# Kernel optimization log

Hardware: AMD Instinct MI355X
Metric: run time of the kernel (lower is better)

Reference implementation:

```python
import jax, jax.numpy as jnp
import numpy as np

HIDDEN = 1152
N_HEADS = 4
N_KV = 1
HEAD_DIM = 256
EPS = 1e-6
B, S = 4, 2048
ROPE_THETA = 1000000.0


def _rms_norm(x, w):
    # x: [..., D] float32; Gemma-style (1 + w) scale
    xf = x.astype(jnp.float32)
    inv = jax.lax.rsqrt(jnp.mean(xf * xf, axis=-1, keepdims=True) + EPS)
    return (xf * inv * (1.0 + w.astype(jnp.float32))).astype(x.dtype)


def _apply_rope(x, cos, sin):
    # x: [B, H, S, D]; cos/sin: [S, D/2]
    d2 = x.shape[-1] // 2
    x1, x2 = x[..., :d2], x[..., d2:]
    cos = cos[None, None, :, :]
    sin = sin[None, None, :, :]
    xr = x1 * cos - x2 * sin
    xi = x1 * sin + x2 * cos
    return jnp.concatenate([xr, xi], axis=-1).astype(x.dtype)


def setup_inputs() -> dict:
    key = jax.random.key(0)
    k_h, k_qkv, k_qn, k_kn, k_o = jax.random.split(key, 5)
    hidden_states = jax.random.normal(k_h, (B, S, HIDDEN), dtype=jnp.float32)
    # causal additive mask [1,1,S,S]
    neg = jnp.finfo(jnp.float32).min
    causal = jnp.tril(jnp.ones((S, S), dtype=bool))
    attention_mask = jnp.where(causal, 0.0, neg)[None, None, :, :].astype(jnp.float32)
    # RoPE tables (complex freqs_cis split into cos/sin)
    inv_freq = 1.0 / (ROPE_THETA ** (np.arange(0, HEAD_DIM, 2, dtype=np.float32) / HEAD_DIM))
    ang = np.arange(S, dtype=np.float32)[:, None] * inv_freq[None, :]
    freqs_cos = jnp.asarray(np.cos(ang))
    freqs_sin = jnp.asarray(np.sin(ang))
    qkv_out = (N_HEADS + 2 * N_KV) * HEAD_DIM
    scale = HIDDEN ** -0.5
    w_qkv = jax.random.normal(k_qkv, (HIDDEN, qkv_out), dtype=jnp.float32) * scale
    w_o = jax.random.normal(k_o, (N_HEADS * HEAD_DIM, HIDDEN), dtype=jnp.float32) * (N_HEADS * HEAD_DIM) ** -0.5
    q_norm_w = jax.random.normal(k_qn, (HEAD_DIM,), dtype=jnp.float32) * 0.02
    k_norm_w = jax.random.normal(k_kn, (HEAD_DIM,), dtype=jnp.float32) * 0.02
    return {
        "hidden_states": hidden_states,
        "attention_mask": attention_mask,
        "freqs_cos": freqs_cos,
        "freqs_sin": freqs_sin,
        "w_qkv": w_qkv,
        "q_norm_w": q_norm_w,
        "k_norm_w": k_norm_w,
        "w_o": w_o,
    }


def reference(hidden_states, attention_mask, freqs_cos, freqs_sin, w_qkv, q_norm_w, k_norm_w, w_o):
    b, s, _ = hidden_states.shape
    groups = N_HEADS // N_KV
    scaling = HEAD_DIM ** -0.5

    qkv = jnp.einsum("bsh,ho->bso", hidden_states, w_qkv)
    q_end = N_HEADS * HEAD_DIM
    k_end = q_end + N_KV * HEAD_DIM
    q = qkv[:, :, :q_end].reshape(b, s, N_HEADS, HEAD_DIM).transpose(0, 2, 1, 3)
    k = qkv[:, :, q_end:k_end].reshape(b, s, N_KV, HEAD_DIM).transpose(0, 2, 1, 3)
    v = qkv[:, :, k_end:].reshape(b, s, N_KV, HEAD_DIM).transpose(0, 2, 1, 3)

    q = _rms_norm(q, q_norm_w)
    k = _rms_norm(k, k_norm_w)

    q = _apply_rope(q, freqs_cos, freqs_sin)
    k = _apply_rope(k, freqs_cos, freqs_sin)

    if groups > 1:
        k = jnp.repeat(k, groups, axis=1)  # [B, H, S, D]
        v = jnp.repeat(v, groups, axis=1)

    scores = jnp.einsum("bhqd,bhkd->bhqk", q * scaling, k)
    scores = scores + attention_mask.astype(jnp.float32)
    probs = jax.nn.softmax(scores.astype(jnp.float32), axis=-1).astype(q.dtype)

    attn = jnp.einsum("bhqk,bhkd->bhqd", probs, v)
    attn = attn.transpose(0, 2, 1, 3).reshape(b, s, N_HEADS * HEAD_DIM)
    return jnp.einsum("bsf,fh->bsh", attn, w_o)
```

## Files before the change

### kernel.cpp

```cpp
#include <hip/hip_runtime.h>

typedef _Float16 f16;
typedef _Float16 f16x8 __attribute__((ext_vector_type(8)));
typedef _Float16 f16x4 __attribute__((ext_vector_type(4)));
typedef float f32x4 __attribute__((ext_vector_type(4)));

#define NH 4
#define HD 256
#define BB 4
#define SS 2048
#define HID 1152
#define QKV_N 1536
#define ODIM (NH * HD)

#define QKV16_OFF 0L
#define HID16_OFF 25165824L
#define OBUF_OFF 0L
#define OPART_OFF 16777216L
#define ML_OFF 44040192L
#define QB_OFF 50331648L
#define KB_OFF 67108864L
#define VT_OFF 71303168L
#define WQKVT_OFF 75497472L
#define WOT_OFF 79036416L

#define GLL16(gp, lp)                                                      \
  __builtin_amdgcn_global_load_lds(                                       \
      (const __attribute__((address_space(1))) char*)(gp),                \
      (__attribute__((address_space(3))) char*)(lp), 16, 0, 0)

__global__ __launch_bounds__(256) void cvt_f32_to_f16(
    const float* __restrict__ s, f16* __restrict__ d, long n) {
  long i = ((long)blockIdx.x * 256 + threadIdx.x) * 8;
  long stride = (long)gridDim.x * 256 * 8;
  for (; i < n; i += stride) {
    float4 a = *(const float4*)(s + i);
    float4 b = *(const float4*)(s + i + 4);
    f16x8 h = {(f16)a.x, (f16)a.y, (f16)a.z, (f16)a.w,
               (f16)b.x, (f16)b.y, (f16)b.z, (f16)b.w};
    *(f16x8*)(d + i) = h;
  }
}

template <typename ST>
__global__ __launch_bounds__(256) void transpose_cvt(
    const ST* __restrict__ src, long src_ld, long src_bs,
    f16* __restrict__ dst, long dst_ld, long dst_bs) {
  __shared__ float tile[32][33];
  src += (long)blockIdx.z * src_bs;
  dst += (long)blockIdx.z * dst_bs;
  int r0 = blockIdx.y * 32, c0 = blockIdx.x * 32;
  int tc = threadIdx.x & 31, tr = threadIdx.x >> 5;
#pragma unroll
  for (int i = 0; i < 4; ++i)
    tile[tr + i * 8][tc] = (float)src[(long)(r0 + tr + i * 8) * src_ld + c0 + tc];
  __syncthreads();
#pragma unroll
  for (int i = 0; i < 4; ++i)
    dst[(long)(c0 + tr + i * 8) * dst_ld + r0 + tc] = (f16)tile[tc][tr + i * 8];
}

template <typename CT>
__global__ __launch_bounds__(256, 3) void gemm_f16(
    const f16* __restrict__ A, const f16* __restrict__ Bt,
    CT* __restrict__ C, int K, int N) {
  __shared__ f16 As[128][64];
  __shared__ f16 Bs[128][64];
  int tid = threadIdx.x, wave = tid >> 6, lane = tid & 63;
  int l16 = lane & 15, lhi = lane >> 4;
  int wm = (wave >> 1) * 64, wn = (wave & 1) * 64;
  long bm = (long)blockIdx.x * 128, bn = (long)blockIdx.y * 128;
  f32x4 acc[4][4] = {};

  int srow = wave * 32 + (lane >> 3);
  int scol = (lane & 7) * 8;
  const f16* Ag = A + (bm + srow) * (long)K + scol;
  const f16* Bg = Bt + (bn + srow) * (long)K + scol;

  for (int k0 = 0; k0 < K; k0 += 64) {
#pragma unroll
    for (int i = 0; i < 4; ++i)
      GLL16(Ag + k0 + (long)i * 8 * K, &As[wave * 32 + i * 8][0]);
#pragma unroll
    for (int i = 0; i < 4; ++i)
      GLL16(Bg + k0 + (long)i * 8 * K, &Bs[wave * 32 + i * 8][0]);
    __syncthreads();
#pragma unroll
    for (int kb = 0; kb < 2; ++kb) {
      f16x8 af[4], bf[4];
#pragma unroll
      for (int i = 0; i < 4; ++i)
        af[i] = *(const f16x8*)&As[wm + i * 16 + l16][kb * 32 + lhi * 8];
#pragma unroll
      for (int j = 0; j < 4; ++j)
        bf[j] = *(const f16x8*)&Bs[wn + j * 16 + l16][kb * 32 + lhi * 8];
#pragma unroll
      for (int i = 0; i < 4; ++i)
#pragma unroll
        for (int j = 0; j < 4; ++j)
          acc[i][j] =
              __builtin_amdgcn_mfma_f32_16x16x32_f16(bf[j], af[i], acc[i][j], 0, 0, 0);
    }
    __syncthreads();
  }

#pragma unroll
  for (int i = 0; i < 4; ++i) {
    long m = bm + wm + i * 16 + l16;
#pragma unroll
    for (int j = 0; j < 4; ++j) {
      long n = bn + wn + j * 16 + lhi * 4;
      if constexpr (sizeof(CT) == 2) {
        f16x4 h = {(f16)acc[i][j][0], (f16)acc[i][j][1], (f16)acc[i][j][2],
                   (f16)acc[i][j][3]};
        *(f16x4*)&C[m * N + n] = h;
      } else {
        *(f32x4*)&C[m * N + n] = acc[i][j];
      }
    }
  }
}

__device__ __forceinline__ void norm_rope_store(
    const f16* __restrict__ x, const float* __restrict__ w,
    const float* __restrict__ fc, const float* __restrict__ fs,
    f16* __restrict__ dst, float scale, int lane) {
  float x0 = (float)x[lane], x1 = (float)x[lane + 64];
  float x2 = (float)x[lane + 128], x3 = (float)x[lane + 192];
  float ss = x0 * x0 + x1 * x1 + x2 * x2 + x3 * x3;
#pragma unroll
  for (int m = 1; m < 64; m <<= 1) ss += __shfl_xor(ss, m, 64);
  float inv = rsqrtf(ss * (1.0f / 256.0f) + 1e-6f);
  x0 *= inv * (1.0f + w[lane]);
  x1 *= inv * (1.0f + w[lane + 64]);
  x2 *= inv * (1.0f + w[lane + 128]);
  x3 *= inv * (1.0f + w[lane + 192]);
  float c0 = fc[lane], s0 = fs[lane], c1 = fc[lane + 64], s1 = fs[lane + 64];
  dst[lane]       = (f16)((x0 * c0 - x2 * s0) * scale);
  dst[lane + 64]  = (f16)((x1 * c1 - x3 * s1) * scale);
  dst[lane + 128] = (f16)((x0 * s0 + x2 * c0) * scale);
  dst[lane + 192] = (f16)((x1 * s1 + x3 * c1) * scale);
}

__global__ __launch_bounds__(256) void qkv_post(
    const f16* __restrict__ qkv, const float* __restrict__ qnw,
    const float* __restrict__ knw, const float* __restrict__ fcos,
    const float* __restrict__ fsin, f16* __restrict__ Q, f16* __restrict__ Kb) {
  long row = blockIdx.x;
  int b = (int)(row >> 11), s = (int)(row & 2047);
  int wave = threadIdx.x >> 6, lane = threadIdx.x & 63;
  const f16* base = qkv + row * QKV_N;
  const float* fc = fcos + (long)s * 128;
  const float* fs = fsin + (long)s * 128;
  norm_rope_store(base + wave * HD, qnw, fc, fs,
                  Q + ((long)(b * NH + wave) * SS + s) * HD, 0.0625f, lane);
  if (wave == 0)
    norm_rope_store(base + NH * HD, knw, fc, fs, Kb + row * HD, 1.0f, lane);
}

__global__ __launch_bounds__(256, 4) void attn_fwd(
    const f16* __restrict__ Q, const f16* __restrict__ Kb,
    const f16* __restrict__ Vt, f16* __restrict__ O,
    f16* __restrict__ Opart, float2* __restrict__ ml) {
  __shared__ f16 Klds[32 * 256];
  __shared__ f16 Vlds[256 * 32];
  __shared__ f16 Plds[4][16][40];
  int bid = blockIdx.x;
  int xcd = bid & 7, slotid = bid >> 3;
  int b = xcd >> 1, par = xcd & 1;
  int h = slotid >> 5, ithalf = slotid & 31;
  int it = ithalf * 2 + par;
  if (it >= 63) return;

  int qb, t0, t1, slot = 0;
  bool split;
  if (it < 11) {
    qb = it; t0 = 0; t1 = 2 * qb + 2; split = false;
  } else {
    int j = it - 11, c, nch, lbase;
    if (j < 22) {
      qb = 11 + (j >> 1); c = j & 1; nch = 2; lbase = (qb - 11) * 2;
    } else {
      int jj = j - 22, q3 = jj / 3;
      qb = 22 + q3; c = jj - q3 * 3; nch = 3; lbase = 22 + q3 * 3;
    }
    int tiles = 2 * qb + 2;
    t0 = tiles * c / nch;
    t1 = tiles * (c + 1) / nch;
    split = true;
    slot = (b * NH + h) * 52 + lbase + c;
  }
  int tid = threadIdx.x, wave = tid >> 6, lane = tid & 63;
  int l16 = lane & 15, lhi = lane >> 4;
  int q0 = qb * 64 + wave * 16;

  const f16* Kg = Kb + (long)b * SS * HD;
  const f16* Vg = Vt + (long)b * HD * SS;

  f16x8 qf[8];
  const f16* Qbase = Q + ((long)(b * NH + h) * SS + q0 + l16) * HD + lhi * 8;
#pragma unroll
  for (int kb = 0; kb < 8; ++kb) qf[kb] = *(const f16x8*)(Qbase + kb * 32);

  f32x4 o[16] = {};
  float m_i = -1e30f, l_i = 0.f;

  int kr = tid >> 5, kc16 = (tid & 31) * 16;
  int rv = tid >> 2, vc16 = (tid & 3) * 16;
  char* kls = (char*)Klds;
  char* vls = (char*)Vlds;
  int kwsw = kc16 ^ (kr << 4);
  int vwsw = vc16 ^ ((rv & 3) << 4);
  const char* krd = kls + l16 * 512;
  int kswz = (l16 & 7) << 4;
  const char* vrd = vls + l16 * 64 + ((lhi * 16) ^ ((l16 & 3) << 4));

  for (int t = t0; t < t1; ++t) {
    long kv0 = (long)t * 32;
    __syncthreads();
#pragma unroll
    for (int i = 0; i < 4; ++i) {
      uint4 kval = *(const uint4*)((const char*)(Kg + (kv0 + kr + 8 * i) * HD) + kc16);
      *(uint4*)(kls + (kr + 8 * i) * 512 + kwsw) = kval;
    }
#pragma unroll
    for (int i = 0; i < 4; ++i) {
      uint4 vval = *(const uint4*)((const char*)(Vg + (long)(rv + 64 * i) * SS + kv0) + vc16);
      *(uint4*)(vls + (rv + 64 * i) * 64 + vwsw) = vval;
    }
    __syncthreads();

    f32x4 sc[2] = {};
    __builtin_amdgcn_s_setprio(1);
#pragma unroll
    for (int kb = 0; kb < 8; ++kb) {
#pragma unroll
      for (int cf = 0; cf < 2; ++cf) {
        f16x8 kf = *(const f16x8*)(krd + cf * 8192 + ((kb * 64 + lhi * 16) ^ kswz));
        sc[cf] = __builtin_amdgcn_mfma_f32_16x16x32_f16(kf, qf[kb], sc[cf], 0, 0, 0);
      }
    }
    __builtin_amdgcn_s_setprio(0);

    float p[8];
    float mx = -1e30f;
    int qrow = q0 + l16;
    if (t >= 2 * qb) {
#pragma unroll
      for (int cf = 0; cf < 2; ++cf)
#pragma unroll
        for (int r = 0; r < 4; ++r) {
          int kv = (int)kv0 + cf * 16 + lhi * 4 + r;
          float s = (kv <= qrow) ? sc[cf][r] : -1e30f;
          p[cf * 4 + r] = s;
          mx = fmaxf(mx, s);
        }
    } else {
#pragma unroll
      for (int i = 0; i < 8; ++i) {
        float s = sc[i >> 2][i & 3];
        p[i] = s;
        mx = fmaxf(mx, s);
      }
    }
    mx = fmaxf(mx, __shfl_xor(mx, 16));
    mx = fmaxf(mx, __shfl_xor(mx, 32));
    float mn = fmaxf(m_i, mx);
    float scl = __expf(m_i - mn);
    float rs = 0.f;
#pragma unroll
    for (int i = 0; i < 8; ++i) {
      p[i] = __expf(p[i] - mn);
      rs += p[i];
    }
    rs += __shfl_xor(rs, 16);
    rs += __shfl_xor(rs, 32);
    l_i = l_i * scl + rs;
    m_i = mn;

#pragma unroll
    for (int cf = 0; cf < 2; ++cf) {
      f16x4 hp = {(f16)p[cf * 4], (f16)p[cf * 4 + 1], (f16)p[cf * 4 + 2],
                  (f16)p[cf * 4 + 3]};
      *(f16x4*)&Plds[wave][l16][cf * 16 + lhi * 4] = hp;
    }

    float s0 = __shfl(scl, lhi * 4 + 0);
    float s1 = __shfl(scl, lhi * 4 + 1);
    float s2 = __shfl(scl, lhi * 4 + 2);
    float s3 = __shfl(scl, lhi * 4 + 3);
#pragma unroll
    for (int nf = 0; nf < 16; ++nf) {
      o[nf][0] *= s0;
      o[nf][1] *= s1;
      o[nf][2] *= s2;
      o[nf][3] *= s3;
    }

    f16x8 pa = *(const f16x8*)&Plds[wave][l16][lhi * 8];
    __builtin_amdgcn_s_setprio(1);
#pragma unroll
    for (int nf = 0; nf < 16; ++nf) {
      f16x8 vf = *(const f16x8*)(vrd + nf * 1024);
      o[nf] = __builtin_amdgcn_mfma_f32_16x16x32_f16(pa, vf, o[nf], 0, 0, 0);
    }
    __builtin_amdgcn_s_setprio(0);
  }

  float inv = 1.0f / l_i;
  float i0 = __shfl(inv, lhi * 4 + 0);
  float i1 = __shfl(inv, lhi * 4 + 1);
  float i2 = __shfl(inv, lhi * 4 + 2);
  float i3 = __shfl(inv, lhi * 4 + 3);
  float ir[4] = {i0, i1, i2, i3};
  if (!split) {
#pragma unroll
    for (int r = 0; r < 4; ++r) {
      long srow = q0 + lhi * 4 + r;
      f16* Orow = O + ((long)b * SS + srow) * ODIM + h * HD + l16;
#pragma unroll
      for (int nf = 0; nf < 16; ++nf) Orow[nf * 16] = (f16)(o[nf][r] * ir[r]);
    }
  } else {
#pragma unroll
    for (int r = 0; r < 4; ++r) {
      int rloc = wave * 16 + lhi * 4 + r;
      f16* Prow = Opart + ((long)slot * 64 + rloc) * HD + l16;
#pragma unroll
      for (int nf = 0; nf < 16; ++nf) Prow[nf * 16] = (f16)(o[nf][r] * ir[r]);
    }
    if (lane < 16) {
      float2 v; v.x = m_i; v.y = l_i;
      ml[(long)slot * 64 + wave * 16 + lane] = v;
    }
  }
}

__global__ __launch_bounds__(256) void attn_combine(
    const f16* __restrict__ Opart, const float2* __restrict__ ml,
    f16* __restrict__ O) {
  int x = blockIdx.x, h = blockIdx.y, b = blockIdx.z;
  int qb = 11 + x;
  int nch = (qb < 22) ? 2 : 3;
  int lbase = (qb < 22) ? (qb - 11) * 2 : 22 + (qb - 22) * 3;
  long slot0 = (long)(b * NH + h) * 52 + lbase;
  int tid = threadIdx.x;
  int r = tid >> 2, d0 = (tid & 3) * 64;
  float m[3], l[3], w[3];
  float M = -1e30f;
#pragma unroll
  for (int c = 0; c < 3; ++c)
    if (c < nch) {
      float2 v = ml[(slot0 + c) * 64 + r];
      m[c] = v.x; l[c] = v.y;
      M = fmaxf(M, v.x);
    }
  float sum = 0.f;
#pragma unroll
  for (int c = 0; c < 3; ++c)
    if (c < nch) { w[c] = l[c] * __expf(m[c] - M); sum += w[c]; }
  float inv = 1.0f / sum;
#pragma unroll
  for (int c = 0; c < 3; ++c)
    if (c < nch) w[c] *= inv;
  f16* Orow = O + ((long)b * SS + qb * 64 + r) * ODIM + h * HD + d0;
#pragma unroll
  for (int i = 0; i < 8; ++i) {
    float acc[8] = {};
#pragma unroll
    for (int c = 0; c < 3; ++c)
      if (c < nch) {
        f16x8 xv = *(const f16x8*)(Opart + ((slot0 + c) * 64 + r) * HD + d0 + i * 8);
#pragma unroll
        for (int j = 0; j < 8; ++j) acc[j] += w[c] * (float)xv[j];
      }
    f16x8 z;
#pragma unroll
    for (int j = 0; j < 8; ++j) z[j] = (f16)acc[j];
    *(f16x8*)(Orow + i * 8) = z;
  }
}

extern "C" void kernel_launch(void* const* d_in, const int* in_sizes, int n_in,
                              void* d_out, int out_size, void* d_ws, size_t ws_size,
                              hipStream_t stream) {
  const float* hidden = (const float*)d_in[0];
  const float* fcos = (const float*)d_in[2];
  const float* fsin = (const float*)d_in[3];
  const float* wqkv = (const float*)d_in[4];
  const float* qnw = (const float*)d_in[5];
  const float* knw = (const float*)d_in[6];
  const float* wo = (const float*)d_in[7];
  float* out = (float*)d_out;

  char* ws = (char*)d_ws;
  f16* qkv16 = (f16*)(ws + QKV16_OFF);
  f16* hid16 = (f16*)(ws + HID16_OFF);
  f16* Obuf = (f16*)(ws + OBUF_OFF);
  f16* Opart = (f16*)(ws + OPART_OFF);
  float2* ml = (float2*)(ws + ML_OFF);
  f16* Qb = (f16*)(ws + QB_OFF);
  f16* Kb = (f16*)(ws + KB_OFF);
  f16* Vt = (f16*)(ws + VT_OFF);
  f16* wqkvt = (f16*)(ws + WQKVT_OFF);
  f16* wot = (f16*)(ws + WOT_OFF);

  cvt_f32_to_f16<<<2048, 256, 0, stream>>>(hidden, hid16, (long)BB * SS * HID);

  transpose_cvt<float><<<dim3(QKV_N / 32, HID / 32, 1), 256, 0, stream>>>(
      wqkv, QKV_N, 0, wqkvt, HID, 0);
  transpose_cvt<float><<<dim3(HID / 32, ODIM / 32, 1), 256, 0, stream>>>(
      wo, HID, 0, wot, ODIM, 0);

  gemm_f16<f16><<<dim3(BB * SS / 128, QKV_N / 128), 256, 0, stream>>>(
      hid16, wqkvt, qkv16, HID, QKV_N);

  qkv_post<<<dim3(BB * SS), 256, 0, stream>>>(qkv16, qnw, knw, fcos, fsin, Qb, Kb);

  transpose_cvt<f16><<<dim3(HD / 32, SS / 32, BB), 256, 0, stream>>>(
      qkv16 + 1280, QKV_N, (long)SS * QKV_N, Vt, SS, (long)HD * SS);

  attn_fwd<<<dim3(1024), 256, 0, stream>>>(Qb, Kb, Vt, Obuf, Opart, ml);
  attn_combine<<<dim3(21, NH, BB), 256, 0, stream>>>(Opart, ml, Obuf);

  gemm_f16<float><<<dim3(BB * SS / 128, HID / 128), 256, 0, stream>>>(
      Obuf, wot, out, ODIM, HID);
}
```

Measured before the change: 240.6 us.

## Load V fragments directly from global into registers and skip rescale when max stable

Removes the V shared-memory staging tile. Each wave now loads its V MFMA operands straight from global memory into registers, issued in two halves so the loads overlap the QK and softmax work. It also adds a lazy-rescale path: if no row's new max exceeds the running max by more than 8, the exponentials reuse the old max and the output accumulator rescale is skipped. The trade-off is that every wave now reads the full V tile from global/L2 redundantly (4x traffic), register pressure rises, and the deferred-max path tolerates exponent values up to e^8 in the fp16 P values.

```diff
diff --git a/kernel.cpp b/kernel.cpp
--- a/kernel.cpp
+++ b/kernel.cpp
@@ -163,7 +163,6 @@
     const f16* __restrict__ Vt, f16* __restrict__ O,
     f16* __restrict__ Opart, float2* __restrict__ ml) {
   __shared__ f16 Klds[32 * 256];
-  __shared__ f16 Vlds[256 * 32];
   __shared__ f16 Plds[4][16][40];
   int bid = blockIdx.x;
   int xcd = bid & 7, slotid = bid >> 3;
@@ -206,14 +205,11 @@
   float m_i = -1e30f, l_i = 0.f;
 
   int kr = tid >> 5, kc16 = (tid & 31) * 16;
-  int rv = tid >> 2, vc16 = (tid & 3) * 16;
   char* kls = (char*)Klds;
-  char* vls = (char*)Vlds;
   int kwsw = kc16 ^ (kr << 4);
-  int vwsw = vc16 ^ ((rv & 3) << 4);
   const char* krd = kls + l16 * 512;
   int kswz = (l16 & 7) << 4;
-  const char* vrd = vls + l16 * 64 + ((lhi * 16) ^ ((l16 & 3) << 4));
+  const f16* vfb = Vg + (long)l16 * SS + lhi * 8;
 
   for (int t = t0; t < t1; ++t) {
     long kv0 = (long)t * 32;
@@ -223,12 +219,12 @@
       uint4 kval = *(const uint4*)((const char*)(Kg + (kv0 + kr + 8 * i) * HD) + kc16);
       *(uint4*)(kls + (kr + 8 * i) * 512 + kwsw) = kval;
     }
-#pragma unroll
-    for (int i = 0; i < 4; ++i) {
-      uint4 vval = *(const uint4*)((const char*)(Vg + (long)(rv + 64 * i) * SS + kv0) + vc16);
-      *(uint4*)(vls + (rv + 64 * i) * 64 + vwsw) = vval;
-    }
     __syncthreads();
+
+    uint4 vr0[8], vr1[8];
+#pragma unroll
+    for (int nf = 0; nf < 8; ++nf)
+      vr0[nf] = *(const uint4*)(vfb + (long)nf * 16 * SS + kv0);
 
     f32x4 sc[2] = {};
     __builtin_amdgcn_s_setprio(1);
@@ -265,18 +261,42 @@
     }
     mx = fmaxf(mx, __shfl_xor(mx, 16));
     mx = fmaxf(mx, __shfl_xor(mx, 32));
-    float mn = fmaxf(m_i, mx);
-    float scl = __expf(m_i - mn);
-    float rs = 0.f;
-#pragma unroll
-    for (int i = 0; i < 8; ++i) {
-      p[i] = __expf(p[i] - mn);
-      rs += p[i];
-    }
-    rs += __shfl_xor(rs, 16);
-    rs += __shfl_xor(rs, 32);
-    l_i = l_i * scl + rs;
-    m_i = mn;
+
+    if (__all(mx <= m_i + 8.f)) {
+      float rs = 0.f;
+#pragma unroll
+      for (int i = 0; i < 8; ++i) {
+        p[i] = __expf(p[i] - m_i);
+        rs += p[i];
+      }
+      rs += __shfl_xor(rs, 16);
+      rs += __shfl_xor(rs, 32);
+      l_i += rs;
+    } else {
+      float mn = fmaxf(m_i, mx);
+      float scl = __expf(m_i - mn);
+      float rs = 0.f;
+#pragma unroll
+      for (int i = 0; i < 8; ++i) {
+        p[i] = __expf(p[i] - mn);
+        rs += p[i];
+      }
+      rs += __shfl_xor(rs, 16);
+      rs += __shfl_xor(rs, 32);
+      l_i = l_i * scl + rs;
+      m_i = mn;
+      float s0 = __shfl(scl, lhi * 4 + 0);
+      float s1 = __shfl(scl, lhi * 4 + 1);
+      float s2 = __shfl(scl, lhi * 4 + 2);
+      float s3 = __shfl(scl, lhi * 4 + 3);
+#pragma unroll
+      for (int nf = 0; nf < 16; ++nf) {
+        o[nf][0] *= s0;
+        o[nf][1] *= s1;
+        o[nf][2] *= s2;
+        o[nf][3] *= s3;
+      }
+    }
 
 #pragma unroll
     for (int cf = 0; cf < 2; ++cf) {
@@ -285,24 +305,21 @@
       *(f16x4*)&Plds[wave][l16][cf * 16 + lhi * 4] = hp;
     }
 
-    float s0 = __shfl(scl, lhi * 4 + 0);
-    float s1 = __shfl(scl, lhi * 4 + 1);
-    float s2 = __shfl(scl, lhi * 4 + 2);
-    float s3 = __shfl(scl, lhi * 4 + 3);
-#pragma unroll
-    for (int nf = 0; nf < 16; ++nf) {
-      o[nf][0] *= s0;
-      o[nf][1] *= s1;
-      o[nf][2] *= s2;
-      o[nf][3] *= s3;
-    }
+#pragma unroll
+    for (int nf = 0; nf < 8; ++nf)
+      vr1[nf] = *(const uint4*)(vfb + (long)(nf + 8) * 16 * SS + kv0);
 
     f16x8 pa = *(const f16x8*)&Plds[wave][l16][lhi * 8];
     __builtin_amdgcn_s_setprio(1);
 #pragma unroll
-    for (int nf = 0; nf < 16; ++nf) {
-      f16x8 vf = *(const f16x8*)(vrd + nf * 1024);
+    for (int nf = 0; nf < 8; ++nf) {
+      f16x8 vf = *(const f16x8*)&vr0[nf];
       o[nf] = __builtin_amdgcn_mfma_f32_16x16x32_f16(pa, vf, o[nf], 0, 0, 0);
+    }
+#pragma unroll
+    for (int nf = 0; nf < 8; ++nf) {
+      f16x8 vf = *(const f16x8*)&vr1[nf];
+      o[nf + 8] = __builtin_amdgcn_mfma_f32_16x16x32_f16(pa, vf, o[nf + 8], 0, 0, 0);
     }
     __builtin_amdgcn_s_setprio(0);
   }
```

Result: slower. 762.5 us (+216.9%).
